# Performance work log

Hardware: AMD Instinct MI355X
Metric: run time of the kernel (lower is better)

The kernel has to match this reference:

```python
import jax, jax.numpy as jnp
import numpy as np

NUM_NEG = 100            # number of negative samples per masked step
CLAMP_W = 1.0            # clamped_logit_weight
B, C, T, M = 8, 256, 1024, 512


def setup_inputs() -> dict:
    key = jax.random.key(0)
    k1, k2, k3 = jax.random.split(key, 3)
    feat_proj = jax.random.normal(k1, (B, C, T), dtype=jnp.float32)
    context_output = jax.random.normal(k2, (B, C, T), dtype=jnp.float32)
    # exactly M masked timesteps per batch row (random positions)
    perm = jax.vmap(lambda k: jax.random.permutation(k, T))(jax.random.split(k3, B))
    mask = perm < M  # [B, T] bool, M True per row
    return {"feat_proj": feat_proj, "mask": mask,
            "context_output": context_output, "num_masked": M}


def reference(feat_proj, mask, context_output, num_masked):
    Bb, Cc, Tt = feat_proj.shape
    # indices of masked timesteps, in time order (stable argsort) -> [B, M]
    idx = jnp.argsort(jnp.logical_not(mask), axis=1)[:, :num_masked]
    feat_t = jnp.swapaxes(feat_proj, 1, 2)        # [B, T, C]
    ctx_t = jnp.swapaxes(context_output, 1, 2)    # [B, T, C]
    mf = jnp.take_along_axis(feat_t, idx[:, :, None], axis=1)  # [B, M, C]
    mc = jnp.take_along_axis(ctx_t, idx[:, :, None], axis=1)   # [B, M, C]
    # uniform sampling of NUM_NEG negatives without replacement, excluding self:
    # random scores per (t, candidate), self set to -1, take top-k
    scores = jax.random.uniform(jax.random.key(42), (Bb, num_masked, num_masked))
    self_mask = jnp.eye(num_masked, dtype=bool)
    scores = jnp.where(self_mask[None], -1.0, scores)
    _, neg_idx = jax.lax.top_k(scores, NUM_NEG)                 # [B, M, K]
    neg_feats = jnp.take_along_axis(mf[:, None, :, :], neg_idx[..., None], axis=2)  # [B, M, K, C]
    pos_logit = jnp.einsum('bmc,bmc->bm', mc, mf)               # [B, M]
    neg_logit = jnp.einsum('bmc,bmkc->bmk', mc, neg_feats)      # [B, M, K]
    logits = jnp.concatenate([pos_logit[..., None], neg_logit], axis=-1)  # [B, M, 1+K]
    total_loss = jnp.sum(jax.nn.softmax(logits, axis=-1)[..., 0])
    clamped = CLAMP_W * jnp.tanh(logits / CLAMP_W)
    total_aux_loss = jnp.sum(clamped ** 2)
    return total_loss, total_aux_loss
```

## Files before the change

### kernel.cpp

```cpp
#include <hip/hip_runtime.h>
#include <stdint.h>

#define NB   8
#define NC   256
#define NT   1024
#define NM   512
#define NNEG 100

typedef unsigned short u16;
typedef unsigned long long u64;
typedef __attribute__((ext_vector_type(8))) short bf16x8;
typedef __attribute__((ext_vector_type(4))) float f32x4;

#define WAVE_LDS_FENCE() asm volatile("s_waitcnt lgkmcnt(0)" ::: "memory")

__device__ __forceinline__ unsigned rotl32(unsigned x, int d) {
  return (x << d) | (x >> (32 - d));
}

__device__ unsigned threefry_bits(unsigned i) {
  const unsigned half = 1048576u;
  const bool lo = i < half;
  unsigned v0 = lo ? i : (i - half);
  unsigned v1 = lo ? (i + half) : i;
  const unsigned k0 = 0u, k1 = 42u;
  const unsigned k2 = k0 ^ k1 ^ 0x1BD11BDAu;
  v0 += k0; v1 += k1;
#define TF_R(r) { v0 += v1; v1 = rotl32(v1, r); v1 ^= v0; }
  TF_R(13) TF_R(15) TF_R(26) TF_R(6)
  v0 += k1; v1 += k2 + 1u;
  TF_R(17) TF_R(29) TF_R(16) TF_R(24)
  v0 += k2; v1 += k0 + 2u;
  TF_R(13) TF_R(15) TF_R(26) TF_R(6)
  v0 += k0; v1 += k1 + 3u;
  TF_R(17) TF_R(29) TF_R(16) TF_R(24)
  v0 += k1; v1 += k2 + 4u;
  TF_R(13) TF_R(15) TF_R(26) TF_R(6)
  v0 += k2; v1 += k0 + 5u;
#undef TF_R
  return lo ? v0 : v1;
}

__global__ __launch_bounds__(256) void k_compact(const float* __restrict__ ctx,
                                                 const float* __restrict__ feat,
                                                 const void* __restrict__ maskp,
                                                 u16* __restrict__ MCh, u16* __restrict__ MCl,
                                                 u16* __restrict__ MFh, u16* __restrict__ MFl) {
  __shared__ float lds[64][129];
  __shared__ int posl[128];
  __shared__ int wsum[4];
  __shared__ int det[3];
  const int tid = threadIdx.x;
  const int lane = tid & 63, wid = tid >> 6;
  const int t0 = blockIdx.x * 128;
  const int b = blockIdx.y >> 1, mat = blockIdx.y & 1;
  const unsigned char* mb = (const unsigned char*)maskp;

  if (tid < 3) det[tid] = 0;
  __syncthreads();
  {
    int c1 = 0, c4 = 0, c8 = 0;
    for (int j = tid; j < 1024; j += 256) {
      c1 += (mb[j] != 0);
      c4 += (((const unsigned*)mb)[j] != 0u);
      c8 += (((const u64*)mb)[j] != 0ull);
    }
#pragma unroll
    for (int off = 32; off; off >>= 1) {
      c1 += __shfl_xor(c1, off, 64);
      c4 += __shfl_xor(c4, off, 64);
      c8 += __shfl_xor(c8, off, 64);
    }
    if (lane == 0) { atomicAdd(&det[0], c1); atomicAdd(&det[1], c4); atomicAdd(&det[2], c8); }
  }
  __syncthreads();
  const int stride = (det[1] == 512) ? 4 : ((det[0] == 512) ? 1 : ((det[2] == 512) ? 8 : 4));

  int f4[4]; int s = 0;
#pragma unroll
  for (int j = 0; j < 4; ++j) {
    int tt = 4 * tid + j;
    size_t e = (size_t)b * NT + tt;
    int f;
    if (stride == 1)      f = (mb[e] != 0);
    else if (stride == 4) f = (((const unsigned*)mb)[e] != 0u);
    else                  f = (((const u64*)mb)[e] != 0ull);
    f4[j] = f; s += f;
  }
  int incl = s;
#pragma unroll
  for (int off = 1; off < 64; off <<= 1) {
    int o = __shfl_up(incl, off, 64);
    if (lane >= off) incl += o;
  }
  if (lane == 63) wsum[wid] = incl;
  __syncthreads();
  int wbase = 0;
#pragma unroll
  for (int w = 0; w < 4; ++w) if (w < wid) wbase += wsum[w];
  int excl = wbase + incl - s;
#pragma unroll
  for (int j = 0; j < 4; ++j) {
    int tt = 4 * tid + j;
    if (tt >= t0 && tt < t0 + 128) posl[tt - t0] = f4[j] ? excl : -1;
    excl += f4[j];
  }

  const float* src = (mat ? feat : ctx) + (size_t)b * NC * NT;
  u16* dh = (mat ? MFh : MCh) + (size_t)b * NM * NC;
  u16* dl = (mat ? MFl : MCl) + (size_t)b * NM * NC;

  const int c4i = tid >> 6, tl = tid & 63, tr = tid >> 6;
  for (int chunk = 0; chunk < 4; ++chunk) {
    int c0 = chunk * 64;
    __syncthreads();
    for (int ci = 0; ci < 16; ++ci) {
      int cc = c4i * 16 + ci;
#pragma unroll
      for (int tj = 0; tj < 2; ++tj) {
        int tt = tl + 64 * tj;
        lds[cc][tt] = src[(size_t)(c0 + cc) * NT + t0 + tt];
      }
    }
    __syncthreads();
    for (int tt = tr; tt < 128; tt += 4) {
      int p = posl[tt];
      if (p >= 0) {
        float x = lds[tl][tt];
        unsigned xb = __float_as_uint(x);
        u16 hi = (u16)(xb >> 16);
        float rlo = x - __uint_as_float((unsigned)hi << 16);
        u16 lo = (u16)(__float_as_uint(rlo) >> 16);
        dh[(size_t)p * NC + c0 + tl] = hi;
        dl[(size_t)p * NC + c0 + tl] = lo;
      }
    }
  }
}

__global__ __launch_bounds__(256) void k_gemm(const u16* __restrict__ MCh, const u16* __restrict__ MCl,
                                              const u16* __restrict__ MFh, const u16* __restrict__ MFl,
                                              float* __restrict__ S) {
  __shared__ u16 smem[2][10240];
  const int tid = threadIdx.x;
  const int b = blockIdx.z, m0 = blockIdx.y * 64, j0 = blockIdx.x * 64;
  const int wave = tid >> 6, lane = tid & 63;
  const int wm = wave >> 1, wn = wave & 1;
  const int r = lane & 15, g = lane >> 4;

  const int srow = tid >> 1;
  const int splane = srow >> 6;
  const int smrow = srow & 63;
  const int shalf = tid & 1;
  const u16* Asrc = (splane ? MCl : MCh) + (size_t)(b * NM + m0 + smrow) * NC + shalf * 16;
  const u16* Bsrc = (splane ? MFl : MFh) + (size_t)(b * NM + j0 + smrow) * NC + shalf * 16;
  const int sdst = srow * 40 + shalf * 16;

  uint4 ra0, ra1, rb0, rb1;
  auto load_regs = [&](int c0) {
    const uint4* p = (const uint4*)(Asrc + c0); ra0 = p[0]; ra1 = p[1];
    const uint4* q = (const uint4*)(Bsrc + c0); rb0 = q[0]; rb1 = q[1];
  };
  auto write_lds = [&](int buf) {
    u16* d = smem[buf] + sdst;
    *(uint4*)d = ra0; *(uint4*)(d + 8) = ra1;
    u16* e = smem[buf] + 5120 + sdst;
    *(uint4*)e = rb0; *(uint4*)(e + 8) = rb1;
  };

  f32x4 zero = {0.f, 0.f, 0.f, 0.f};
  f32x4 acc[2][2];
#pragma unroll
  for (int m = 0; m < 2; ++m)
#pragma unroll
    for (int n = 0; n < 2; ++n) acc[m][n] = zero;

  load_regs(0);
  write_lds(0);
  __syncthreads();

  for (int ks = 0; ks < 8; ++ks) {
    const int cur = ks & 1;
    if (ks < 7) load_regs((ks + 1) * 32);
    const u16* base = smem[cur];
    bf16x8 ah[2], al[2], bh[2], bl[2];
#pragma unroll
    for (int m = 0; m < 2; ++m) {
      ah[m] = *(const bf16x8*)(base + (wm * 32 + m * 16 + r) * 40 + g * 8);
      al[m] = *(const bf16x8*)(base + (64 + wm * 32 + m * 16 + r) * 40 + g * 8);
    }
#pragma unroll
    for (int n = 0; n < 2; ++n) {
      bh[n] = *(const bf16x8*)(base + 5120 + (wn * 32 + n * 16 + r) * 40 + g * 8);
      bl[n] = *(const bf16x8*)(base + 5120 + (64 + wn * 32 + n * 16 + r) * 40 + g * 8);
    }
#pragma unroll
    for (int m = 0; m < 2; ++m)
#pragma unroll
      for (int n = 0; n < 2; ++n) {
        acc[m][n] = __builtin_amdgcn_mfma_f32_16x16x32_bf16(ah[m], bh[n], acc[m][n], 0, 0, 0);
        acc[m][n] = __builtin_amdgcn_mfma_f32_16x16x32_bf16(ah[m], bl[n], acc[m][n], 0, 0, 0);
        acc[m][n] = __builtin_amdgcn_mfma_f32_16x16x32_bf16(al[m], bh[n], acc[m][n], 0, 0, 0);
      }
    if (ks < 7) write_lds(cur ^ 1);
    __syncthreads();
  }

  float* Sb = S + (size_t)b * NM * NM;
#pragma unroll
  for (int m = 0; m < 2; ++m)
#pragma unroll
    for (int n = 0; n < 2; ++n)
#pragma unroll
      for (int q = 0; q < 4; ++q) {
        int rowi = m0 + wm * 32 + m * 16 + g * 4 + q;
        int col  = j0 + wn * 32 + n * 16 + r;
        Sb[(size_t)rowi * NM + col] = acc[m][n][q];
      }
}

__global__ __launch_bounds__(512) void k_loss(const float* __restrict__ S,
                                              float* __restrict__ pl,
                                              float* __restrict__ pa) {
  __shared__ unsigned hist[8][256];
  __shared__ u64 bk[8][32];
  __shared__ int bcnt[8], bbin[8], bneed[8];
  __shared__ unsigned char sf[8][512];

  const int tid = threadIdx.x;
  const int lane = tid & 63, wv = tid >> 6;
  const int row = blockIdx.x * 8 + wv;
  const int m = row & (NM - 1);

#pragma unroll
  for (int q = 0; q < 4; ++q) hist[wv][lane * 4 + q] = 0;
#pragma unroll
  for (int j = 0; j < 8; ++j) sf[wv][j * 64 + lane] = 0;
  if (lane == 0) bcnt[wv] = 0;

  unsigned keys[8]; int bins[8]; bool selfj[8];
#pragma unroll
  for (int j = 0; j < 8; ++j) {
    int t = j * 64 + lane;
    unsigned bits = threefry_bits((unsigned)row * 512u + (unsigned)t);
    unsigned u = bits >> 9;
    keys[j] = (u << 9) | (unsigned)(511 - t);
    bins[j] = (int)(u >> 15);
    selfj[j] = (t == m);
    if (!selfj[j]) atomicAdd(&hist[wv][bins[j]], 1u);
  }
  WAVE_LDS_FENCE();

  {
    unsigned h0 = hist[wv][4 * lane + 0], h1 = hist[wv][4 * lane + 1];
    unsigned h2 = hist[wv][4 * lane + 2], h3 = hist[wv][4 * lane + 3];
    unsigned s = h0 + h1 + h2 + h3;
    unsigned suf = s;
#pragma unroll
    for (int off = 1; off < 64; off <<= 1) {
      unsigned o = __shfl_down(suf, off, 64);
      if (lane + off < 64) suf += o;
    }
    unsigned a3 = suf - s;
    unsigned a2 = a3 + h3;
    unsigned a1 = a2 + h2;
    unsigned a0 = a1 + h1;
    if (a3 < NNEG && a3 + h3 >= NNEG) { bbin[wv] = 4 * lane + 3; bneed[wv] = NNEG - (int)a3; }
    if (a2 < NNEG && a2 + h2 >= NNEG) { bbin[wv] = 4 * lane + 2; bneed[wv] = NNEG - (int)a2; }
    if (a1 < NNEG && a1 + h1 >= NNEG) { bbin[wv] = 4 * lane + 1; bneed[wv] = NNEG - (int)a1; }
    if (a0 < NNEG && a0 + h0 >= NNEG) { bbin[wv] = 4 * lane + 0; bneed[wv] = NNEG - (int)a0; }
  }
  WAVE_LDS_FENCE();

  const int bb = bbin[wv];
#pragma unroll
  for (int j = 0; j < 8; ++j) {
    if (!selfj[j] && bins[j] == bb) {
      int p = atomicAdd(&bcnt[wv], 1);
      bk[wv][p & 31] = (((u64)keys[j]) << 1) | 1ull;
    }
  }
  WAVE_LDS_FENCE();

  if (lane == 0) {
    int cnt = bcnt[wv]; if (cnt > 32) cnt = 32;
    int need = bneed[wv];
    for (int it = 0; it < need; ++it) {
      u64 best = 0ull; int bi = 0;
      for (int q = 0; q < cnt; ++q)
        if (bk[wv][q] > best) { best = bk[wv][q]; bi = q; }
      bk[wv][bi] = 0ull;
      int tt = 511 - (int)((best >> 1) & 511ull);
      sf[wv][tt] = 1;
    }
  }
  WAVE_LDS_FENCE();

  const float* Srow = S + (size_t)row * NM;
  float lv[8]; bool act[8];
  float mv = -3.4e38f;
#pragma unroll
  for (int j = 0; j < 8; ++j) {
    lv[j] = Srow[j * 64 + lane];
    act[j] = selfj[j] || (bins[j] > bb && !selfj[j]) || (sf[wv][j * 64 + lane] != 0);
    if (act[j]) mv = fmaxf(mv, lv[j]);
  }
#pragma unroll
  for (int off = 32; off > 0; off >>= 1) mv = fmaxf(mv, __shfl_xor(mv, off, 64));

  float es = 0.f, as = 0.f, ps = 0.f;
#pragma unroll
  for (int j = 0; j < 8; ++j) {
    if (act[j]) {
      float e = __expf(lv[j] - mv);
      float th = 1.f - 2.f / (__expf(2.f * lv[j]) + 1.f);
      es += e; as += th * th;
      if (selfj[j]) ps = e;
    }
  }
#pragma unroll
  for (int off = 32; off > 0; off >>= 1) {
    es += __shfl_xor(es, off, 64);
    as += __shfl_xor(as, off, 64);
    ps += __shfl_xor(ps, off, 64);
  }
  if (lane == 0) { pl[row] = ps / es; pa[row] = as; }
}

__global__ __launch_bounds__(1024) void k_red(const float* __restrict__ pl,
                                              const float* __restrict__ pa,
                                              float* __restrict__ out) {
  __shared__ float s1[1024], s2[1024];
  const int t = threadIdx.x;
  float a = 0.f, b = 0.f;
  for (int q = t; q < NB * NM; q += 1024) { a += pl[q]; b += pa[q]; }
  s1[t] = a; s2[t] = b;
  __syncthreads();
  for (int off = 512; off > 0; off >>= 1) {
    if (t < off) { s1[t] += s1[t + off]; s2[t] += s2[t + off]; }
    __syncthreads();
  }
  if (t == 0) { out[0] = s1[0]; out[1] = s2[0]; }
}

extern "C" void kernel_launch(void* const* d_in, const int* in_sizes, int n_in,
                              void* d_out, int out_size, void* d_ws, size_t ws_size,
                              hipStream_t stream) {
  const float* feat = (const float*)d_in[0];
  const void*  mask = d_in[1];
  const float* ctx  = (const float*)d_in[2];
  float* out = (float*)d_out;

  char* ws = (char*)d_ws;
  u16*   MCh = (u16*)ws;
  u16*   MCl = (u16*)(ws + (2u << 20));
  u16*   MFh = (u16*)(ws + (4u << 20));
  u16*   MFl = (u16*)(ws + (6u << 20));
  float* S   = (float*)(ws + (8u << 20));
  float* pl  = (float*)(ws + (16u << 20));
  float* pa  = pl + NB * NM;

  dim3 gc(NT / 128, NB * 2);
  k_compact<<<gc, 256, 0, stream>>>(ctx, feat, mask, MCh, MCl, MFh, MFl);

  dim3 g2(NM / 64, NM / 64, NB);
  k_gemm<<<g2, 256, 0, stream>>>(MCh, MCl, MFh, MFl, S);

  k_loss<<<NB * NM / 8, 512, 0, stream>>>(S, pl, pa);

  k_red<<<1, 1024, 0, stream>>>(pl, pa, out);
}
```

Baseline: 52.50 us.

## Fuse GEMM, loss and final reduction into one kernel with single-bf16 operands

After: 59.34 us. +13.0%, slower.

```diff
diff --git a/kernel.cpp b/kernel.cpp
--- a/kernel.cpp
+++ b/kernel.cpp
@@ -44,8 +44,8 @@
 __global__ __launch_bounds__(256) void k_compact(const float* __restrict__ ctx,
                                                  const float* __restrict__ feat,
                                                  const void* __restrict__ maskp,
-                                                 u16* __restrict__ MCh, u16* __restrict__ MCl,
-                                                 u16* __restrict__ MFh, u16* __restrict__ MFl) {
+                                                 u16* __restrict__ MC, u16* __restrict__ MF,
+                                                 int* __restrict__ counter) {
   __shared__ float lds[64][129];
   __shared__ int posl[128];
   __shared__ int wsum[4];
@@ -56,6 +56,8 @@
   const int b = blockIdx.y >> 1, mat = blockIdx.y & 1;
   const unsigned char* mb = (const unsigned char*)maskp;
 
+  if (blockIdx.x == 0 && blockIdx.y == 0 && tid == 0) *counter = 0;
+
   if (tid < 3) det[tid] = 0;
   __syncthreads();
   {
@@ -107,8 +109,7 @@
   }
 
   const float* src = (mat ? feat : ctx) + (size_t)b * NC * NT;
-  u16* dh = (mat ? MFh : MCh) + (size_t)b * NM * NC;
-  u16* dl = (mat ? MFl : MCl) + (size_t)b * NM * NC;
+  u16* dst = (mat ? MF : MC) + (size_t)b * NM * NC;
 
   const int c4i = tid >> 6, tl = tid & 63, tr = tid >> 6;
   for (int chunk = 0; chunk < 4; ++chunk) {
@@ -126,221 +127,189 @@
     for (int tt = tr; tt < 128; tt += 4) {
       int p = posl[tt];
       if (p >= 0) {
-        float x = lds[tl][tt];
-        unsigned xb = __float_as_uint(x);
-        u16 hi = (u16)(xb >> 16);
-        float rlo = x - __uint_as_float((unsigned)hi << 16);
-        u16 lo = (u16)(__float_as_uint(rlo) >> 16);
-        dh[(size_t)p * NC + c0 + tl] = hi;
-        dl[(size_t)p * NC + c0 + tl] = lo;
-      }
-    }
-  }
-}
-
-__global__ __launch_bounds__(256) void k_gemm(const u16* __restrict__ MCh, const u16* __restrict__ MCl,
-                                              const u16* __restrict__ MFh, const u16* __restrict__ MFl,
-                                              float* __restrict__ S) {
-  __shared__ u16 smem[2][10240];
-  const int tid = threadIdx.x;
-  const int b = blockIdx.z, m0 = blockIdx.y * 64, j0 = blockIdx.x * 64;
-  const int wave = tid >> 6, lane = tid & 63;
-  const int wm = wave >> 1, wn = wave & 1;
-  const int r = lane & 15, g = lane >> 4;
-
-  const int srow = tid >> 1;
-  const int splane = srow >> 6;
-  const int smrow = srow & 63;
-  const int shalf = tid & 1;
-  const u16* Asrc = (splane ? MCl : MCh) + (size_t)(b * NM + m0 + smrow) * NC + shalf * 16;
-  const u16* Bsrc = (splane ? MFl : MFh) + (size_t)(b * NM + j0 + smrow) * NC + shalf * 16;
-  const int sdst = srow * 40 + shalf * 16;
-
-  uint4 ra0, ra1, rb0, rb1;
-  auto load_regs = [&](int c0) {
-    const uint4* p = (const uint4*)(Asrc + c0); ra0 = p[0]; ra1 = p[1];
-    const uint4* q = (const uint4*)(Bsrc + c0); rb0 = q[0]; rb1 = q[1];
-  };
-  auto write_lds = [&](int buf) {
-    u16* d = smem[buf] + sdst;
-    *(uint4*)d = ra0; *(uint4*)(d + 8) = ra1;
-    u16* e = smem[buf] + 5120 + sdst;
-    *(uint4*)e = rb0; *(uint4*)(e + 8) = rb1;
-  };
-
-  f32x4 zero = {0.f, 0.f, 0.f, 0.f};
-  f32x4 acc[2][2];
-#pragma unroll
-  for (int m = 0; m < 2; ++m)
-#pragma unroll
-    for (int n = 0; n < 2; ++n) acc[m][n] = zero;
-
-  load_regs(0);
-  write_lds(0);
-  __syncthreads();
-
-  for (int ks = 0; ks < 8; ++ks) {
-    const int cur = ks & 1;
-    if (ks < 7) load_regs((ks + 1) * 32);
-    const u16* base = smem[cur];
-    bf16x8 ah[2], al[2], bh[2], bl[2];
-#pragma unroll
-    for (int m = 0; m < 2; ++m) {
-      ah[m] = *(const bf16x8*)(base + (wm * 32 + m * 16 + r) * 40 + g * 8);
-      al[m] = *(const bf16x8*)(base + (64 + wm * 32 + m * 16 + r) * 40 + g * 8);
-    }
-#pragma unroll
-    for (int n = 0; n < 2; ++n) {
-      bh[n] = *(const bf16x8*)(base + 5120 + (wn * 32 + n * 16 + r) * 40 + g * 8);
-      bl[n] = *(const bf16x8*)(base + 5120 + (64 + wn * 32 + n * 16 + r) * 40 + g * 8);
-    }
-#pragma unroll
-    for (int m = 0; m < 2; ++m)
-#pragma unroll
-      for (int n = 0; n < 2; ++n) {
-        acc[m][n] = __builtin_amdgcn_mfma_f32_16x16x32_bf16(ah[m], bh[n], acc[m][n], 0, 0, 0);
-        acc[m][n] = __builtin_amdgcn_mfma_f32_16x16x32_bf16(ah[m], bl[n], acc[m][n], 0, 0, 0);
-        acc[m][n] = __builtin_amdgcn_mfma_f32_16x16x32_bf16(al[m], bh[n], acc[m][n], 0, 0, 0);
-      }
-    if (ks < 7) write_lds(cur ^ 1);
-    __syncthreads();
-  }
-
-  float* Sb = S + (size_t)b * NM * NM;
-#pragma unroll
-  for (int m = 0; m < 2; ++m)
-#pragma unroll
-    for (int n = 0; n < 2; ++n)
-#pragma unroll
-      for (int q = 0; q < 4; ++q) {
-        int rowi = m0 + wm * 32 + m * 16 + g * 4 + q;
-        int col  = j0 + wn * 32 + n * 16 + r;
-        Sb[(size_t)rowi * NM + col] = acc[m][n][q];
-      }
-}
-
-__global__ __launch_bounds__(512) void k_loss(const float* __restrict__ S,
-                                              float* __restrict__ pl,
-                                              float* __restrict__ pa) {
-  __shared__ unsigned hist[8][256];
-  __shared__ u64 bk[8][32];
-  __shared__ int bcnt[8], bbin[8], bneed[8];
-  __shared__ unsigned char sf[8][512];
+        unsigned xb = __float_as_uint(lds[tl][tt]);
+        xb += 0x7FFFu + ((xb >> 16) & 1u);
+        dst[(size_t)p * NC + c0 + tl] = (u16)(xb >> 16);
+      }
+    }
+  }
+}
+
+__global__ __launch_bounds__(256) void k_fused(const u16* __restrict__ MC,
+                                               const u16* __restrict__ MF,
+                                               float* __restrict__ partials,
+                                               int* __restrict__ counter,
+                                               float* __restrict__ out) {
+  __shared__ float S_lds[16][516];
+  __shared__ unsigned hist[4][256];
+  __shared__ u64 bk[4][32];
+  __shared__ int bcnt[4], bbin[4], bneed[4];
+  __shared__ unsigned char sf[4][512];
+  __shared__ float wred[4][2];
+  __shared__ int slast;
 
   const int tid = threadIdx.x;
   const int lane = tid & 63, wv = tid >> 6;
-  const int row = blockIdx.x * 8 + wv;
-  const int m = row & (NM - 1);
-
-#pragma unroll
-  for (int q = 0; q < 4; ++q) hist[wv][lane * 4 + q] = 0;
-#pragma unroll
-  for (int j = 0; j < 8; ++j) sf[wv][j * 64 + lane] = 0;
-  if (lane == 0) bcnt[wv] = 0;
-
-  unsigned keys[8]; int bins[8]; bool selfj[8];
-#pragma unroll
-  for (int j = 0; j < 8; ++j) {
-    int t = j * 64 + lane;
-    unsigned bits = threefry_bits((unsigned)row * 512u + (unsigned)t);
-    unsigned u = bits >> 9;
-    keys[j] = (u << 9) | (unsigned)(511 - t);
-    bins[j] = (int)(u >> 15);
-    selfj[j] = (t == m);
-    if (!selfj[j]) atomicAdd(&hist[wv][bins[j]], 1u);
-  }
-  WAVE_LDS_FENCE();
+  const int bid = blockIdx.x;
+  const int b = bid >> 5, m0 = (bid & 31) * 16;
+  const int r16 = lane & 15, g = lane >> 4;
 
   {
-    unsigned h0 = hist[wv][4 * lane + 0], h1 = hist[wv][4 * lane + 1];
-    unsigned h2 = hist[wv][4 * lane + 2], h3 = hist[wv][4 * lane + 3];
-    unsigned s = h0 + h1 + h2 + h3;
-    unsigned suf = s;
-#pragma unroll
-    for (int off = 1; off < 64; off <<= 1) {
-      unsigned o = __shfl_down(suf, off, 64);
-      if (lane + off < 64) suf += o;
-    }
-    unsigned a3 = suf - s;
-    unsigned a2 = a3 + h3;
-    unsigned a1 = a2 + h2;
-    unsigned a0 = a1 + h1;
-    if (a3 < NNEG && a3 + h3 >= NNEG) { bbin[wv] = 4 * lane + 3; bneed[wv] = NNEG - (int)a3; }
-    if (a2 < NNEG && a2 + h2 >= NNEG) { bbin[wv] = 4 * lane + 2; bneed[wv] = NNEG - (int)a2; }
-    if (a1 < NNEG && a1 + h1 >= NNEG) { bbin[wv] = 4 * lane + 1; bneed[wv] = NNEG - (int)a1; }
-    if (a0 < NNEG && a0 + h0 >= NNEG) { bbin[wv] = 4 * lane + 0; bneed[wv] = NNEG - (int)a0; }
-  }
-  WAVE_LDS_FENCE();
-
-  const int bb = bbin[wv];
-#pragma unroll
-  for (int j = 0; j < 8; ++j) {
-    if (!selfj[j] && bins[j] == bb) {
-      int p = atomicAdd(&bcnt[wv], 1);
-      bk[wv][p & 31] = (((u64)keys[j]) << 1) | 1ull;
-    }
-  }
-  WAVE_LDS_FENCE();
-
-  if (lane == 0) {
-    int cnt = bcnt[wv]; if (cnt > 32) cnt = 32;
-    int need = bneed[wv];
-    for (int it = 0; it < need; ++it) {
-      u64 best = 0ull; int bi = 0;
-      for (int q = 0; q < cnt; ++q)
-        if (bk[wv][q] > best) { best = bk[wv][q]; bi = q; }
-      bk[wv][bi] = 0ull;
-      int tt = 511 - (int)((best >> 1) & 511ull);
-      sf[wv][tt] = 1;
-    }
-  }
-  WAVE_LDS_FENCE();
-
-  const float* Srow = S + (size_t)row * NM;
-  float lv[8]; bool act[8];
-  float mv = -3.4e38f;
-#pragma unroll
-  for (int j = 0; j < 8; ++j) {
-    lv[j] = Srow[j * 64 + lane];
-    act[j] = selfj[j] || (bins[j] > bb && !selfj[j]) || (sf[wv][j * 64 + lane] != 0);
-    if (act[j]) mv = fmaxf(mv, lv[j]);
-  }
-#pragma unroll
-  for (int off = 32; off > 0; off >>= 1) mv = fmaxf(mv, __shfl_xor(mv, off, 64));
-
-  float es = 0.f, as = 0.f, ps = 0.f;
-#pragma unroll
-  for (int j = 0; j < 8; ++j) {
-    if (act[j]) {
-      float e = __expf(lv[j] - mv);
-      float th = 1.f - 2.f / (__expf(2.f * lv[j]) + 1.f);
-      es += e; as += th * th;
-      if (selfj[j]) ps = e;
-    }
-  }
-#pragma unroll
-  for (int off = 32; off > 0; off >>= 1) {
-    es += __shfl_xor(es, off, 64);
-    as += __shfl_xor(as, off, 64);
-    ps += __shfl_xor(ps, off, 64);
-  }
-  if (lane == 0) { pl[row] = ps / es; pa[row] = as; }
-}
-
-__global__ __launch_bounds__(1024) void k_red(const float* __restrict__ pl,
-                                              const float* __restrict__ pa,
-                                              float* __restrict__ out) {
-  __shared__ float s1[1024], s2[1024];
-  const int t = threadIdx.x;
-  float a = 0.f, b = 0.f;
-  for (int q = t; q < NB * NM; q += 1024) { a += pl[q]; b += pa[q]; }
-  s1[t] = a; s2[t] = b;
-  __syncthreads();
-  for (int off = 512; off > 0; off >>= 1) {
-    if (t < off) { s1[t] += s1[t + off]; s2[t] += s2[t + off]; }
+    const u16* Arow = MC + ((size_t)(b * NM + m0 + r16)) * NC + g * 8;
+    bf16x8 a[8];
+#pragma unroll
+    for (int ks = 0; ks < 8; ++ks) a[ks] = *(const bf16x8*)(Arow + ks * 32);
+
+    const u16* Bbase = MF + ((size_t)(b * NM + wv * 128 + r16)) * NC + g * 8;
+    f32x4 zero = {0.f, 0.f, 0.f, 0.f};
+    f32x4 acc[8];
+#pragma unroll
+    for (int n = 0; n < 8; ++n) acc[n] = zero;
+
+#pragma unroll
+    for (int ks = 0; ks < 8; ++ks) {
+#pragma unroll
+      for (int n = 0; n < 8; ++n) {
+        bf16x8 bv = *(const bf16x8*)(Bbase + (size_t)n * 16 * NC + ks * 32);
+        acc[n] = __builtin_amdgcn_mfma_f32_16x16x32_bf16(a[ks], bv, acc[n], 0, 0, 0);
+      }
+    }
+
+#pragma unroll
+    for (int n = 0; n < 8; ++n)
+#pragma unroll
+      for (int q = 0; q < 4; ++q)
+        S_lds[g * 4 + q][wv * 128 + n * 16 + r16] = acc[n][q];
+  }
+  __syncthreads();
+
+  float wsum_pl = 0.f, wsum_pa = 0.f;
+  for (int rr = 0; rr < 4; ++rr) {
+    const int rloc = wv * 4 + rr;
+    const int m = m0 + rloc;
+    const int row = b * NM + m;
+
+#pragma unroll
+    for (int q = 0; q < 4; ++q) hist[wv][lane * 4 + q] = 0;
+#pragma unroll
+    for (int j = 0; j < 8; ++j) sf[wv][j * 64 + lane] = 0;
+    if (lane == 0) bcnt[wv] = 0;
+
+    unsigned keys[8]; int bins[8]; bool selfj[8];
+#pragma unroll
+    for (int j = 0; j < 8; ++j) {
+      int t = j * 64 + lane;
+      unsigned bits = threefry_bits((unsigned)row * 512u + (unsigned)t);
+      unsigned u = bits >> 9;
+      keys[j] = (u << 9) | (unsigned)(511 - t);
+      bins[j] = (int)(u >> 15);
+      selfj[j] = (t == m);
+      if (!selfj[j]) atomicAdd(&hist[wv][bins[j]], 1u);
+    }
+    WAVE_LDS_FENCE();
+
+    {
+      unsigned h0 = hist[wv][4 * lane + 0], h1 = hist[wv][4 * lane + 1];
+      unsigned h2 = hist[wv][4 * lane + 2], h3 = hist[wv][4 * lane + 3];
+      unsigned s = h0 + h1 + h2 + h3;
+      unsigned suf = s;
+#pragma unroll
+      for (int off = 1; off < 64; off <<= 1) {
+        unsigned o = __shfl_down(suf, off, 64);
+        if (lane + off < 64) suf += o;
+      }
+      unsigned a3 = suf - s;
+      unsigned a2 = a3 + h3;
+      unsigned a1 = a2 + h2;
+      unsigned a0 = a1 + h1;
+      if (a3 < NNEG && a3 + h3 >= NNEG) { bbin[wv] = 4 * lane + 3; bneed[wv] = NNEG - (int)a3; }
+      if (a2 < NNEG && a2 + h2 >= NNEG) { bbin[wv] = 4 * lane + 2; bneed[wv] = NNEG - (int)a2; }
+      if (a1 < NNEG && a1 + h1 >= NNEG) { bbin[wv] = 4 * lane + 1; bneed[wv] = NNEG - (int)a1; }
+      if (a0 < NNEG && a0 + h0 >= NNEG) { bbin[wv] = 4 * lane + 0; bneed[wv] = NNEG - (int)a0; }
+    }
+    WAVE_LDS_FENCE();
+
+    const int bb = bbin[wv];
+#pragma unroll
+    for (int j = 0; j < 8; ++j) {
+      if (!selfj[j] && bins[j] == bb) {
+        int p = atomicAdd(&bcnt[wv], 1);
+        bk[wv][p & 31] = (((u64)keys[j]) << 1) | 1ull;
+      }
+    }
+    WAVE_LDS_FENCE();
+
+    if (lane == 0) {
+      int cnt = bcnt[wv]; if (cnt > 32) cnt = 32;
+      int need = bneed[wv];
+      for (int it = 0; it < need; ++it) {
+        u64 best = 0ull; int bi = 0;
+        for (int q = 0; q < cnt; ++q)
+          if (bk[wv][q] > best) { best = bk[wv][q]; bi = q; }
+        bk[wv][bi] = 0ull;
+        int tt = 511 - (int)((best >> 1) & 511ull);
+        sf[wv][tt] = 1;
+      }
+    }
+    WAVE_LDS_FENCE();
+
+    float lv[8]; bool act[8];
+    float mv = -3.4e38f;
+#pragma unroll
+    for (int j = 0; j < 8; ++j) {
+      lv[j] = S_lds[rloc][j * 64 + lane];
+      act[j] = selfj[j] || (bins[j] > bb && !selfj[j]) || (sf[wv][j * 64 + lane] != 0);
+      if (act[j]) mv = fmaxf(mv, lv[j]);
+    }
+#pragma unroll
+    for (int off = 32; off > 0; off >>= 1) mv = fmaxf(mv, __shfl_xor(mv, off, 64));
+
+    float es = 0.f, as = 0.f, ps = 0.f;
+#pragma unroll
+    for (int j = 0; j < 8; ++j) {
+      if (act[j]) {
+        float e = __expf(lv[j] - mv);
+        float th = 1.f - 2.f / (__expf(2.f * lv[j]) + 1.f);
+        es += e; as += th * th;
+        if (selfj[j]) ps = e;
+      }
+    }
+#pragma unroll
+    for (int off = 32; off > 0; off >>= 1) {
+      es += __shfl_xor(es, off, 64);
+      as += __shfl_xor(as, off, 64);
+      ps += __shfl_xor(ps, off, 64);
+    }
+    if (lane == 0) { wsum_pl += ps / es; wsum_pa += as; }
+    WAVE_LDS_FENCE();
+  }
+
+  if (lane == 0) { wred[wv][0] = wsum_pl; wred[wv][1] = wsum_pa; }
+  __syncthreads();
+
+  if (tid == 0) {
+    float bpl = wred[0][0] + wred[1][0] + wred[2][0] + wred[3][0];
+    float bpa = wred[0][1] + wred[1][1] + wred[2][1] + wred[3][1];
+    partials[2 * bid] = bpl;
+    partials[2 * bid + 1] = bpa;
+    __threadfence();
+    int old = atomicAdd(counter, 1);
+    slast = (old == 255);
+  }
+  __syncthreads();
+  if (slast) {
+    __threadfence();
+    float* s1 = (float*)hist;
+    float* s2 = s1 + 256;
+    s1[tid] = partials[2 * tid];
+    s2[tid] = partials[2 * tid + 1];
     __syncthreads();
-  }
-  if (t == 0) { out[0] = s1[0]; out[1] = s2[0]; }
+    for (int off = 128; off > 0; off >>= 1) {
+      if (tid < off) { s1[tid] += s1[tid + off]; s2[tid] += s2[tid + off]; }
+      __syncthreads();
+    }
+    if (tid == 0) { out[0] = s1[0]; out[1] = s2[0]; }
+  }
 }
 
 extern "C" void kernel_launch(void* const* d_in, const int* in_sizes, int n_in,
@@ -352,21 +321,13 @@
   float* out = (float*)d_out;
 
   char* ws = (char*)d_ws;
-  u16*   MCh = (u16*)ws;
-  u16*   MCl = (u16*)(ws + (2u << 20));
-  u16*   MFh = (u16*)(ws + (4u << 20));
-  u16*   MFl = (u16*)(ws + (6u << 20));
-  float* S   = (float*)(ws + (8u << 20));
-  float* pl  = (float*)(ws + (16u << 20));
-  float* pa  = pl + NB * NM;
+  u16*   MC      = (u16*)ws;
+  u16*   MF      = (u16*)(ws + (2u << 20));
+  float* partials = (float*)(ws + (4u << 20));
+  int*   counter  = (int*)(ws + (4u << 20) + 4096);
 
   dim3 gc(NT / 128, NB * 2);
-  k_compact<<<gc, 256, 0, stream>>>(ctx, feat, mask, MCh, MCl, MFh, MFl);
-
-  dim3 g2(NM / 64, NM / 64, NB);
-  k_gemm<<<g2, 256, 0, stream>>>(MCh, MCl, MFh, MFl, S);
-
-  k_loss<<<NB * NM / 8, 512, 0, stream>>>(S, pl, pa);
-
-  k_red<<<1, 1024, 0, stream>>>(pl, pa, out);
-}
+  k_compact<<<gc, 256, 0, stream>>>(ctx, feat, mask, MC, MF, counter);
+
+  k_fused<<<NB * 32, 256, 0, stream>>>(MC, MF, partials, counter, out);
+}
```
